# Kernel tuning notes

Measured on AMD Instinct MI355X. Metric: run time of the kernel, lower is better.

Reference implementation:

```python
import jax, jax.numpy as jnp
import numpy as np

B, H, L, D, S = 4, 16, 4096, 64, 128

def setup_inputs() -> dict:
    key = jax.random.key(0)
    k1, k2 = jax.random.split(key)
    x = jax.random.normal(k1, (B, H, L, D), dtype=jnp.float32)
    c = jax.random.normal(k2, (H, S, D), dtype=jnp.float32)
    # codebook rows are unit-normalized at init (matches torch init)
    c = c / jnp.linalg.norm(c, axis=-1, keepdims=True)
    return {"x": x, "c": c}

def reference(x, c):
    # cosine-similarity scores: [B,H,L,S]
    cos_sim = jnp.einsum('bhld,hsd->bhls', x, c)
    delta_index = jnp.argmax(cos_sim, axis=-1)            # [B,H,L]
    delta_onehot = jax.nn.one_hot(delta_index, c.shape[-2], dtype=jnp.float32)  # [B,H,L,S]
    return (delta_onehot, c)
```

## Files before the change

kernel.cpp:

```cpp
#include <hip/hip_runtime.h>
#include <hip/hip_bf16.h>
#include <math.h>

constexpr int BB = 4;
constexpr int HH = 16;
constexpr int LL = 4096;
constexpr int DD = 64;
constexpr int SS = 128;
constexpr int BM = 64;


typedef __attribute__((ext_vector_type(8))) short bf16x8;
typedef __attribute__((ext_vector_type(4))) float f32x4;

__device__ __forceinline__ void split3(const float* __restrict__ p,
                                       bf16x8& H8, bf16x8& M8, bf16x8& L8) {
    float v[8];
    *(f32x4*)&v[0] = *(const f32x4*)p;
    *(f32x4*)&v[4] = *(const f32x4*)(p + 4);
    short H[8], M[8], L[8];
    #pragma unroll
    for (int e = 0; e < 8; ++e) {
        const float xv = v[e];
        const unsigned u0 = __float_as_uint(xv);
        const float hf = __uint_as_float(u0 & 0xFFFF0000u);
        const float r1 = xv - hf;
        const unsigned u1 = __float_as_uint(r1);
        const float mf = __uint_as_float(u1 & 0xFFFF0000u);
        const float r2 = r1 - mf;
        const unsigned u2 = __float_as_uint(r2);
        H[e] = (short)(u0 >> 16);
        M[e] = (short)(u1 >> 16);
        L[e] = (short)(u2 >> 16);
    }
    H8 = *(bf16x8*)H; M8 = *(bf16x8*)M; L8 = *(bf16x8*)L;
}

__global__ __launch_bounds__(256, 2) void quantizer_kernel(
    const float* __restrict__ x,
    const float* __restrict__ c,
    float* __restrict__ out,
    float* __restrict__ out_c)
{
    const int tid = threadIdx.x;
    const int blk = blockIdx.x;
    const long long r0 = (long long)blk * BM;
    const int h = (int)((r0 >> 12) & (HH - 1));
    const float* __restrict__ chead = c + (size_t)h * SS * DD;

    const int lane = tid & 63;
    const int wc = tid >> 6;
    const int lm = lane & 15;
    const int q  = lane >> 4;

    f32x4 accB[4][2] = {};
    f32x4 accS[4][2] = {};

    #pragma unroll
    for (int k0 = 0; k0 < DD; k0 += 32) {
        bf16x8 Ah[4], Am[4], Al[4], Bh[2], Bm[2], Bl[2];
        #pragma unroll
        for (int a = 0; a < 4; ++a) {
            const float* p = x + (size_t)(r0 + a * 16 + lm) * DD + k0 + q * 8;
            split3(p, Ah[a], Am[a], Al[a]);
        }
        #pragma unroll
        for (int b = 0; b < 2; ++b) {
            const float* p = chead + (size_t)(wc * 32 + b * 16 + lm) * DD + k0 + q * 8;
            split3(p, Bh[b], Bm[b], Bl[b]);
        }
        #pragma unroll
        for (int a = 0; a < 4; ++a) {
            #pragma unroll
            for (int b = 0; b < 2; ++b) {
                accB[a][b] = __builtin_amdgcn_mfma_f32_16x16x32_bf16(Ah[a], Bh[b], accB[a][b], 0, 0, 0);
                accS[a][b] = __builtin_amdgcn_mfma_f32_16x16x32_bf16(Ah[a], Bm[b], accS[a][b], 0, 0, 0);
                accS[a][b] = __builtin_amdgcn_mfma_f32_16x16x32_bf16(Am[a], Bh[b], accS[a][b], 0, 0, 0);
                accS[a][b] = __builtin_amdgcn_mfma_f32_16x16x32_bf16(Am[a], Bm[b], accS[a][b], 0, 0, 0);
                accS[a][b] = __builtin_amdgcn_mfma_f32_16x16x32_bf16(Ah[a], Bl[b], accS[a][b], 0, 0, 0);
                accS[a][b] = __builtin_amdgcn_mfma_f32_16x16x32_bf16(Al[a], Bh[b], accS[a][b], 0, 0, 0);
                accS[a][b] = __builtin_amdgcn_mfma_f32_16x16x32_bf16(Am[a], Bl[b], accS[a][b], 0, 0, 0);
                accS[a][b] = __builtin_amdgcn_mfma_f32_16x16x32_bf16(Al[a], Bm[b], accS[a][b], 0, 0, 0);
            }
        }
    }

    __shared__ float rval[BM][65];
    __shared__ int   ridx[BM][65];
    __shared__ int   amax[BM];

    const int cg = wc * 16 + lm;
    #pragma unroll
    for (int a = 0; a < 4; ++a) {
        #pragma unroll
        for (int r = 0; r < 4; ++r) {
            const float v0 = accB[a][0][r] + accS[a][0][r];
            const float v1 = accB[a][1][r] + accS[a][1][r];
            const int c0 = wc * 32 + lm;
            const int c1 = wc * 32 + 16 + lm;
            const bool t = (v1 > v0);
            const int row = a * 16 + q * 4 + r;
            rval[row][cg] = t ? v1 : v0;
            ridx[row][cg] = t ? c1 : c0;
        }
    }
    __syncthreads();

    if (tid < BM) {
        float bv = rval[tid][0];
        int bc = ridx[tid][0];
        #pragma unroll 8
        for (int t = 1; t < 64; ++t) {
            const float v = rval[tid][t];
            const int ci = ridx[tid][t];
            if (v > bv || (v == bv && ci < bc)) { bv = v; bc = ci; }
        }
        amax[tid] = bc;
    }
    __syncthreads();

    float4* __restrict__ op = (float4*)(out + (size_t)r0 * SS);
    #pragma unroll
    for (int i = tid; i < BM * (SS / 4); i += 256) {
        const int rr = i >> 5;
        const int s0 = (i & 31) * 4;
        const int am = amax[rr];
        float4 v;
        v.x = (s0 + 0 == am) ? 1.f : 0.f;
        v.y = (s0 + 1 == am) ? 1.f : 0.f;
        v.z = (s0 + 2 == am) ? 1.f : 0.f;
        v.w = (s0 + 3 == am) ? 1.f : 0.f;
        op[i] = v;
    }

    if (blk < 128) {
        const float4* __restrict__ src = (const float4*)c;
        float4* __restrict__ dst = (float4*)out_c;
        const int idx = blk * 256 + tid;
        dst[idx] = src[idx];
    }
}

extern "C" void kernel_launch(void* const* d_in, const int* in_sizes, int n_in,
                              void* d_out, int out_size, void* d_ws, size_t ws_size,
                              hipStream_t stream) {
    const float* x = (const float*)d_in[0];
    const float* c = (const float*)d_in[1];
    float* out = (float*)d_out;
    float* out_c = out + (size_t)BB * HH * LL * SS;

    const int rows = BB * HH * LL;
    const int blocks = rows / BM;
    quantizer_kernel<<<blocks, 256, 0, stream>>>(x, c, out, out_c);
}
```

Measured before the change: 232.3 us.

## Stage bf16-split x and codebook tiles in shared memory once per block

Splits each x row and codebook row into bf16 hi/mid/lo parts once per block and stores them in padded LDS. The MFMA loop then reads its fragments from LDS instead of every wave reloading and re-splitting from global memory. This removes redundant global loads and splitting arithmetic across waves. In exchange it adds an extra barrier and about 80KB of LDS per block, which is reused for the argmax reduction and may limit occupancy.

```diff
diff --git a/kernel.cpp b/kernel.cpp
--- a/kernel.cpp
+++ b/kernel.cpp
@@ -42,11 +42,41 @@
     float* __restrict__ out,
     float* __restrict__ out_c)
 {
+    alignas(16) __shared__ short smem[39936];
+    short* __restrict__ sAh = smem;
+    short* __restrict__ sAm = smem + 4608;
+    short* __restrict__ sAl = smem + 9216;
+    short* __restrict__ sBh = smem + 13312;
+    short* __restrict__ sBm = smem + 22528;
+    short* __restrict__ sBl = smem + 31744;
+
     const int tid = threadIdx.x;
     const int blk = blockIdx.x;
     const long long r0 = (long long)blk * BM;
     const int h = (int)((r0 >> 12) & (HH - 1));
     const float* __restrict__ chead = c + (size_t)h * SS * DD;
+
+    #pragma unroll
+    for (int i = 0; i < 2; ++i) {
+        const int t = tid + i * 256;
+        const int row = t >> 3, oct = t & 7;
+        bf16x8 H, M, L;
+        split3(x + (size_t)(r0 + row) * DD + oct * 8, H, M, L);
+        *(bf16x8*)(sAh + row * 72 + oct * 8) = H;
+        *(bf16x8*)(sAm + row * 72 + oct * 8) = M;
+        *(bf16x8*)(sAl + row * 64 + oct * 8) = L;
+    }
+    #pragma unroll
+    for (int i = 0; i < 4; ++i) {
+        const int t = tid + i * 256;
+        const int code = t >> 3, oct = t & 7;
+        bf16x8 H, M, L;
+        split3(chead + code * DD + oct * 8, H, M, L);
+        *(bf16x8*)(sBh + code * 72 + oct * 8) = H;
+        *(bf16x8*)(sBm + code * 72 + oct * 8) = M;
+        *(bf16x8*)(sBl + code * 64 + oct * 8) = L;
+    }
+    __syncthreads();
 
     const int lane = tid & 63;
     const int wc = tid >> 6;
@@ -58,16 +88,21 @@
 
     #pragma unroll
     for (int k0 = 0; k0 < DD; k0 += 32) {
+        const int kk = k0 + q * 8;
         bf16x8 Ah[4], Am[4], Al[4], Bh[2], Bm[2], Bl[2];
         #pragma unroll
         for (int a = 0; a < 4; ++a) {
-            const float* p = x + (size_t)(r0 + a * 16 + lm) * DD + k0 + q * 8;
-            split3(p, Ah[a], Am[a], Al[a]);
+            const int m = a * 16 + lm;
+            Ah[a] = *(const bf16x8*)(sAh + m * 72 + kk);
+            Am[a] = *(const bf16x8*)(sAm + m * 72 + kk);
+            Al[a] = *(const bf16x8*)(sAl + m * 64 + kk);
         }
         #pragma unroll
         for (int b = 0; b < 2; ++b) {
-            const float* p = chead + (size_t)(wc * 32 + b * 16 + lm) * DD + k0 + q * 8;
-            split3(p, Bh[b], Bm[b], Bl[b]);
+            const int n = wc * 32 + b * 16 + lm;
+            Bh[b] = *(const bf16x8*)(sBh + n * 72 + kk);
+            Bm[b] = *(const bf16x8*)(sBm + n * 72 + kk);
+            Bl[b] = *(const bf16x8*)(sBl + n * 64 + kk);
         }
         #pragma unroll
         for (int a = 0; a < 4; ++a) {
@@ -85,9 +120,10 @@
         }
     }
 
-    __shared__ float rval[BM][65];
-    __shared__ int   ridx[BM][65];
-    __shared__ int   amax[BM];
+    __syncthreads();
+    float* __restrict__ rval = (float*)smem;
+    int*   __restrict__ ridx = (int*)smem + 4160;
+    int*   __restrict__ amax = ridx + 4160;
 
     const int cg = wc * 16 + lm;
     #pragma unroll
@@ -100,19 +136,19 @@
             const int c1 = wc * 32 + 16 + lm;
             const bool t = (v1 > v0);
             const int row = a * 16 + q * 4 + r;
-            rval[row][cg] = t ? v1 : v0;
-            ridx[row][cg] = t ? c1 : c0;
+            rval[row * 65 + cg] = t ? v1 : v0;
+            ridx[row * 65 + cg] = t ? c1 : c0;
         }
     }
     __syncthreads();
 
     if (tid < BM) {
-        float bv = rval[tid][0];
-        int bc = ridx[tid][0];
+        float bv = rval[tid * 65];
+        int bc = ridx[tid * 65];
         #pragma unroll 8
         for (int t = 1; t < 64; ++t) {
-            const float v = rval[tid][t];
-            const int ci = ridx[tid][t];
+            const float v = rval[tid * 65 + t];
+            const int ci = ridx[tid * 65 + t];
             if (v > bv || (v == bv && ci < bc)) { bv = v; bc = ci; }
         }
         amax[tid] = bc;
```

After: 228.5 us. About the same (-1.6%).

## Stage pre-split codebook in shared memory and loop over row tiles per block

Applied to the files above, without the earlier changes.

Each block now handles 512 rows instead of 64. The codebook head is split into three bf16 parts once per block and stored in padded shared memory, rather than being re-split from global memory for every 64-row tile. Each wave computes all 128 codes for its 16 rows, prefetches the next tile's x into registers, and reduces the argmax with wave shuffles instead of a shared-memory pass gated by __syncthreads. This cuts redundant codebook loads and conversion work and removes block-wide syncs, in exchange for 8x fewer blocks, more registers per wave, and a per-wave serial loop.

```diff
diff --git a/kernel.cpp b/kernel.cpp
--- a/kernel.cpp
+++ b/kernel.cpp
@@ -7,17 +7,17 @@
 constexpr int LL = 4096;
 constexpr int DD = 64;
 constexpr int SS = 128;
-constexpr int BM = 64;
+constexpr int NT = 8;
 
 
 typedef __attribute__((ext_vector_type(8))) short bf16x8;
 typedef __attribute__((ext_vector_type(4))) float f32x4;
 
-__device__ __forceinline__ void split3(const float* __restrict__ p,
-                                       bf16x8& H8, bf16x8& M8, bf16x8& L8) {
+__device__ __forceinline__ void split3reg(f32x4 v0, f32x4 v1,
+                                          bf16x8& H8, bf16x8& M8, bf16x8& L8) {
     float v[8];
-    *(f32x4*)&v[0] = *(const f32x4*)p;
-    *(f32x4*)&v[4] = *(const f32x4*)(p + 4);
+    *(f32x4*)&v[0] = v0;
+    *(f32x4*)&v[4] = v1;
     short H[8], M[8], L[8];
     #pragma unroll
     for (int e = 0; e < 8; ++e) {
@@ -42,95 +42,125 @@
     float* __restrict__ out,
     float* __restrict__ out_c)
 {
+    alignas(16) __shared__ short smem[3 * 128 * 80 + 128];
+    short* __restrict__ sBh = smem;
+    short* __restrict__ sBm = smem + 10240;
+    short* __restrict__ sBl = smem + 20480;
+    int*   __restrict__ swx = (int*)(smem + 30720);
+
     const int tid = threadIdx.x;
     const int blk = blockIdx.x;
-    const long long r0 = (long long)blk * BM;
-    const int h = (int)((r0 >> 12) & (HH - 1));
+    const long long r0 = (long long)blk * 512;
+    const int h = (blk >> 3) & (HH - 1);
     const float* __restrict__ chead = c + (size_t)h * SS * DD;
 
+    #pragma unroll
+    for (int i = 0; i < 4; ++i) {
+        const int t = tid + i * 256;
+        const int code = t >> 3, oct = t & 7;
+        const f32x4* cp = (const f32x4*)(chead + code * DD + oct * 8);
+        bf16x8 H, M, L;
+        split3reg(cp[0], cp[1], H, M, L);
+        *(bf16x8*)&sBh[code * 80 + oct * 8] = H;
+        *(bf16x8*)&sBm[code * 80 + oct * 8] = M;
+        *(bf16x8*)&sBl[code * 80 + oct * 8] = L;
+    }
+    __syncthreads();
+
     const int lane = tid & 63;
-    const int wc = tid >> 6;
+    const int w = tid >> 6;
     const int lm = lane & 15;
     const int q  = lane >> 4;
 
-    f32x4 accB[4][2] = {};
-    f32x4 accS[4][2] = {};
+    auto loadraw = [&](long long rw0, f32x4& a0, f32x4& a1, f32x4& b0, f32x4& b1) {
+        const float* p = x + (rw0 + lm) * (long long)DD;
+        a0 = *(const f32x4*)(p + q * 8);
+        a1 = *(const f32x4*)(p + q * 8 + 4);
+        b0 = *(const f32x4*)(p + 32 + q * 8);
+        b1 = *(const f32x4*)(p + 32 + q * 8 + 4);
+    };
 
-    #pragma unroll
-    for (int k0 = 0; k0 < DD; k0 += 32) {
-        bf16x8 Ah[4], Am[4], Al[4], Bh[2], Bm[2], Bl[2];
+    f32x4 ra0, ra1, rb0, rb1;
+    f32x4 na0 = {}, na1 = {}, nb0 = {}, nb1 = {};
+    loadraw(r0 + w * 16, ra0, ra1, rb0, rb1);
+
+    #pragma unroll 1
+    for (int t = 0; t < NT; ++t) {
+        const long long rw0 = r0 + t * 64 + w * 16;
+        if (t + 1 < NT) loadraw(rw0 + 64, na0, na1, nb0, nb1);
+
+        bf16x8 Ah0, Am0, Al0, Ah1, Am1, Al1;
+        split3reg(ra0, ra1, Ah0, Am0, Al0);
+        split3reg(rb0, rb1, Ah1, Am1, Al1);
+
+        f32x4 accB[8] = {};
+        f32x4 accS[8] = {};
         #pragma unroll
-        for (int a = 0; a < 4; ++a) {
-            const float* p = x + (size_t)(r0 + a * 16 + lm) * DD + k0 + q * 8;
-            split3(p, Ah[a], Am[a], Al[a]);
+        for (int b = 0; b < 8; ++b) {
+            const int n = b * 16 + lm;
+            const bf16x8 Bh0 = *(const bf16x8*)&sBh[n * 80 + q * 8];
+            const bf16x8 Bm0 = *(const bf16x8*)&sBm[n * 80 + q * 8];
+            const bf16x8 Bl0 = *(const bf16x8*)&sBl[n * 80 + q * 8];
+            const bf16x8 Bh1 = *(const bf16x8*)&sBh[n * 80 + 32 + q * 8];
+            const bf16x8 Bm1 = *(const bf16x8*)&sBm[n * 80 + 32 + q * 8];
+            const bf16x8 Bl1 = *(const bf16x8*)&sBl[n * 80 + 32 + q * 8];
+            accB[b] = __builtin_amdgcn_mfma_f32_16x16x32_bf16(Ah0, Bh0, accB[b], 0, 0, 0);
+            accB[b] = __builtin_amdgcn_mfma_f32_16x16x32_bf16(Ah1, Bh1, accB[b], 0, 0, 0);
+            accS[b] = __builtin_amdgcn_mfma_f32_16x16x32_bf16(Ah0, Bm0, accS[b], 0, 0, 0);
+            accS[b] = __builtin_amdgcn_mfma_f32_16x16x32_bf16(Am0, Bh0, accS[b], 0, 0, 0);
+            accS[b] = __builtin_amdgcn_mfma_f32_16x16x32_bf16(Am0, Bm0, accS[b], 0, 0, 0);
+            accS[b] = __builtin_amdgcn_mfma_f32_16x16x32_bf16(Ah0, Bl0, accS[b], 0, 0, 0);
+            accS[b] = __builtin_amdgcn_mfma_f32_16x16x32_bf16(Al0, Bh0, accS[b], 0, 0, 0);
+            accS[b] = __builtin_amdgcn_mfma_f32_16x16x32_bf16(Am0, Bl0, accS[b], 0, 0, 0);
+            accS[b] = __builtin_amdgcn_mfma_f32_16x16x32_bf16(Al0, Bm0, accS[b], 0, 0, 0);
+            accS[b] = __builtin_amdgcn_mfma_f32_16x16x32_bf16(Ah1, Bm1, accS[b], 0, 0, 0);
+            accS[b] = __builtin_amdgcn_mfma_f32_16x16x32_bf16(Am1, Bh1, accS[b], 0, 0, 0);
+            accS[b] = __builtin_amdgcn_mfma_f32_16x16x32_bf16(Am1, Bm1, accS[b], 0, 0, 0);
+            accS[b] = __builtin_amdgcn_mfma_f32_16x16x32_bf16(Ah1, Bl1, accS[b], 0, 0, 0);
+            accS[b] = __builtin_amdgcn_mfma_f32_16x16x32_bf16(Al1, Bh1, accS[b], 0, 0, 0);
+            accS[b] = __builtin_amdgcn_mfma_f32_16x16x32_bf16(Am1, Bl1, accS[b], 0, 0, 0);
+            accS[b] = __builtin_amdgcn_mfma_f32_16x16x32_bf16(Al1, Bm1, accS[b], 0, 0, 0);
+        }
+
+        float bv[4]; int bi[4];
+        #pragma unroll
+        for (int r = 0; r < 4; ++r) {
+            bv[r] = accB[0][r] + accS[0][r];
+            bi[r] = lm;
+            #pragma unroll
+            for (int b = 1; b < 8; ++b) {
+                const float v = accB[b][r] + accS[b][r];
+                if (v > bv[r]) { bv[r] = v; bi[r] = b * 16 + lm; }
+            }
         }
         #pragma unroll
-        for (int b = 0; b < 2; ++b) {
-            const float* p = chead + (size_t)(wc * 32 + b * 16 + lm) * DD + k0 + q * 8;
-            split3(p, Bh[b], Bm[b], Bl[b]);
-        }
-        #pragma unroll
-        for (int a = 0; a < 4; ++a) {
+        for (int mask = 1; mask <= 8; mask <<= 1) {
             #pragma unroll
-            for (int b = 0; b < 2; ++b) {
-                accB[a][b] = __builtin_amdgcn_mfma_f32_16x16x32_bf16(Ah[a], Bh[b], accB[a][b], 0, 0, 0);
-                accS[a][b] = __builtin_amdgcn_mfma_f32_16x16x32_bf16(Ah[a], Bm[b], accS[a][b], 0, 0, 0);
-                accS[a][b] = __builtin_amdgcn_mfma_f32_16x16x32_bf16(Am[a], Bh[b], accS[a][b], 0, 0, 0);
-                accS[a][b] = __builtin_amdgcn_mfma_f32_16x16x32_bf16(Am[a], Bm[b], accS[a][b], 0, 0, 0);
-                accS[a][b] = __builtin_amdgcn_mfma_f32_16x16x32_bf16(Ah[a], Bl[b], accS[a][b], 0, 0, 0);
-                accS[a][b] = __builtin_amdgcn_mfma_f32_16x16x32_bf16(Al[a], Bh[b], accS[a][b], 0, 0, 0);
-                accS[a][b] = __builtin_amdgcn_mfma_f32_16x16x32_bf16(Am[a], Bl[b], accS[a][b], 0, 0, 0);
-                accS[a][b] = __builtin_amdgcn_mfma_f32_16x16x32_bf16(Al[a], Bm[b], accS[a][b], 0, 0, 0);
+            for (int r = 0; r < 4; ++r) {
+                const float ov = __shfl_xor(bv[r], mask);
+                const int   oi = __shfl_xor(bi[r], mask);
+                if (ov > bv[r] || (ov == bv[r] && oi < bi[r])) { bv[r] = ov; bi[r] = oi; }
             }
         }
-    }
+        if (lm == 0)
+            *(int4*)&swx[w * 16 + q * 4] = make_int4(bi[0], bi[1], bi[2], bi[3]);
 
-    __shared__ float rval[BM][65];
-    __shared__ int   ridx[BM][65];
-    __shared__ int   amax[BM];
+        float4* __restrict__ op = (float4*)(out + rw0 * SS);
+        #pragma unroll
+        for (int p = 0; p < 8; ++p) {
+            const int row  = p * 2 + (lane >> 5);
+            const int col4 = (p * 64 + lane) & 31;
+            const int am = swx[w * 16 + row];
+            const int s0 = col4 * 4;
+            float4 v;
+            v.x = (s0 + 0 == am) ? 1.f : 0.f;
+            v.y = (s0 + 1 == am) ? 1.f : 0.f;
+            v.z = (s0 + 2 == am) ? 1.f : 0.f;
+            v.w = (s0 + 3 == am) ? 1.f : 0.f;
+            op[row * (SS / 4) + col4] = v;
+        }
 
-    const int cg = wc * 16 + lm;
-    #pragma unroll
-    for (int a = 0; a < 4; ++a) {
-        #pragma unroll
-        for (int r = 0; r < 4; ++r) {
-            const float v0 = accB[a][0][r] + accS[a][0][r];
-            const float v1 = accB[a][1][r] + accS[a][1][r];
-            const int c0 = wc * 32 + lm;
-            const int c1 = wc * 32 + 16 + lm;
-            const bool t = (v1 > v0);
-            const int row = a * 16 + q * 4 + r;
-            rval[row][cg] = t ? v1 : v0;
-            ridx[row][cg] = t ? c1 : c0;
-        }
-    }
-    __syncthreads();
-
-    if (tid < BM) {
-        float bv = rval[tid][0];
-        int bc = ridx[tid][0];
-        #pragma unroll 8
-        for (int t = 1; t < 64; ++t) {
-            const float v = rval[tid][t];
-            const int ci = ridx[tid][t];
-            if (v > bv || (v == bv && ci < bc)) { bv = v; bc = ci; }
-        }
-        amax[tid] = bc;
-    }
-    __syncthreads();
-
-    float4* __restrict__ op = (float4*)(out + (size_t)r0 * SS);
-    #pragma unroll
-    for (int i = tid; i < BM * (SS / 4); i += 256) {
-        const int rr = i >> 5;
-        const int s0 = (i & 31) * 4;
-        const int am = amax[rr];
-        float4 v;
-        v.x = (s0 + 0 == am) ? 1.f : 0.f;
-        v.y = (s0 + 1 == am) ? 1.f : 0.f;
-        v.z = (s0 + 2 == am) ? 1.f : 0.f;
-        v.w = (s0 + 3 == am) ? 1.f : 0.f;
-        op[i] = v;
+        ra0 = na0; ra1 = na1; rb0 = nb0; rb1 = nb1;
     }
 
     if (blk < 128) {
@@ -150,6 +180,6 @@
     float* out_c = out + (size_t)BB * HH * LL * SS;
 
     const int rows = BB * HH * LL;
-    const int blocks = rows / BM;
+    const int blocks = rows / 512;
     quantizer_kernel<<<blocks, 256, 0, stream>>>(x, c, out, out_c);
 }
```

Measured after the change: 233.2 us. Within noise of the previous version (+0.4%).
